# Performance work log

Measured on AMD Instinct MI355X. Metric: run time of the kernel, lower is better.

The kernel has to match this reference:

```python
import jax, jax.numpy as jnp
import numpy as np

DIM = 512
NUM_EXPERTS = 8
HID = 4 * DIM
B, S = 2, 2048


def setup_inputs() -> dict:
    key = jax.random.key(0)
    ks = jax.random.split(key, 7)
    sc = 0.02
    x = jax.random.normal(ks[0], (B, S, DIM), dtype=jnp.float32)
    Wr = jax.random.normal(ks[1], (DIM, NUM_EXPERTS), dtype=jnp.float32) * sc
    br = jnp.zeros((NUM_EXPERTS,), dtype=jnp.float32)
    W1 = jax.random.normal(ks[2], (NUM_EXPERTS, DIM, HID), dtype=jnp.float32) * sc
    b1 = jnp.zeros((NUM_EXPERTS, HID), dtype=jnp.float32)
    W2 = jax.random.normal(ks[3], (NUM_EXPERTS, HID, DIM), dtype=jnp.float32) * sc
    b2 = jnp.zeros((NUM_EXPERTS, DIM), dtype=jnp.float32)
    return {"x": x, "Wr": Wr, "br": br, "W1": W1, "b1": b1, "W2": W2, "b2": b2}


def reference(x, Wr, br, W1, b1, W2, b2):
    b, s, d = x.shape
    E = Wr.shape[1]
    xf = x.reshape(-1, d)                                   # [N, d]
    N = xf.shape[0]
    logits = xf @ Wr + br                                   # [N, E]
    probs = jax.nn.softmax(logits, axis=-1)
    top_w, top_idx = jax.lax.top_k(probs, 2)                # [N, 2]
    top_w = jax.nn.softmax(top_w, axis=-1)                  # renormalize top-2
    # combine weight per (token, expert); topk indices are distinct so add is safe
    comb = jnp.zeros((N, E), dtype=xf.dtype)
    comb = comb.at[jnp.arange(N)[:, None], top_idx].add(top_w)  # [N, E]
    # dense per-expert MLP (eval mode: dropout is identity); exact GELU as nn.GELU
    h = jax.nn.gelu(jnp.einsum('nd,edf->enf', xf, W1) + b1[:, None, :], approximate=False)
    y = jnp.einsum('enf,efd->end', h, W2) + b2[:, None, :]  # [E, N, d]
    out = jnp.einsum('end,ne->nd', y, comb)                 # weighted combine
    # load-balancing loss
    load = jnp.zeros((E,), dtype=jnp.float32).at[top_idx.reshape(-1)].add(1.0)
    load = load / load.sum()
    lb_loss = jnp.sum((load - 1.0 / E) ** 2)
    return out.reshape(b, s, d), lb_loss, load
```

## Files before the change

### kernel.cpp

```cpp
#include <hip/hip_runtime.h>
#include <hip/hip_bf16.h>

#define DIMD 512
#define NEXP 8
#define HIDN 2048
#define NTOK 4096
#define NASG 8192

typedef short bf16x8 __attribute__((ext_vector_type(8)));
typedef float f32x4 __attribute__((ext_vector_type(4)));

__device__ inline unsigned short f2bf(float f) {
  __hip_bfloat16 h = __float2bfloat16(f);
  return __builtin_bit_cast(unsigned short, h);
}

__device__ inline void gl16(const void* g, void* l) {
  __builtin_amdgcn_global_load_lds(
      (const __attribute__((address_space(1))) unsigned int*)g,
      (__attribute__((address_space(3))) unsigned int*)l, 16, 0, 0);
}

#define PIPE_WAIT4_BAR() do { \
  asm volatile("s_waitcnt vmcnt(4)" ::: "memory"); \
  __builtin_amdgcn_s_barrier(); \
  __builtin_amdgcn_sched_barrier(0); } while (0)
#define PIPE_WAIT0_BAR() do { \
  asm volatile("s_waitcnt vmcnt(0)" ::: "memory"); \
  __builtin_amdgcn_s_barrier(); \
  __builtin_amdgcn_sched_barrier(0); } while (0)
#define PIPE_POST_BAR() do { \
  asm volatile("" ::: "memory"); \
  __builtin_amdgcn_sched_barrier(0); \
  __builtin_amdgcn_s_barrier(); } while (0)

__global__ __launch_bounds__(256) void transpose_both_kernel(
    const float* __restrict__ W1, const float* __restrict__ W2,
    unsigned short* __restrict__ w1t, unsigned short* __restrict__ w2t) {
  __shared__ float tile[64][65];
  int z = blockIdx.z;
  int e = z & 7;
  const float* src; unsigned short* dst; int R, C, r0, c0;
  if (z < 8) { src = W1; dst = w1t; R = DIMD; C = HIDN; c0 = blockIdx.x * 64; r0 = blockIdx.y * 64; }
  else       { src = W2; dst = w2t; R = HIDN; C = DIMD; r0 = blockIdx.x * 64; c0 = blockIdx.y * 64; }
  const float* s = src + (size_t)e * R * C;
  unsigned short* d = dst + (size_t)e * R * C;
  for (int i = threadIdx.x; i < 4096; i += 256) {
    int r = i >> 6, c = i & 63;
    tile[r][c] = s[(size_t)(r0 + r) * C + (c0 + c)];
  }
  __syncthreads();
  for (int i = threadIdx.x; i < 2048; i += 256) {
    int c = i >> 5;
    int r = (i & 31) * 2;
    unsigned lo = f2bf(tile[r][c]);
    unsigned hi = f2bf(tile[r + 1][c]);
    *reinterpret_cast<unsigned*>(d + (size_t)(c0 + c) * R + (r0 + r)) = lo | (hi << 16);
  }
}

__global__ __launch_bounds__(256) void router_kernel(const float* __restrict__ x,
                                                     const float* __restrict__ Wr,
                                                     const float* __restrict__ br,
                                                     int* __restrict__ tidx,
                                                     float* __restrict__ tw,
                                                     unsigned short* __restrict__ xb) {
  int lane = threadIdx.x & 63;
  int n = blockIdx.x * 4 + (threadIdx.x >> 6);
  const float* xr = x + (size_t)n * DIMD;
  unsigned short* xbr = xb + (size_t)n * DIMD;
  float acc[NEXP];
#pragma unroll
  for (int e = 0; e < NEXP; ++e) acc[e] = 0.f;
#pragma unroll
  for (int it = 0; it < 2; ++it) {
    int d0 = it * 256 + lane * 4;
    float4 xv = *reinterpret_cast<const float4*>(xr + d0);
    unsigned p0 = (unsigned)f2bf(xv.x) | ((unsigned)f2bf(xv.y) << 16);
    unsigned p1 = (unsigned)f2bf(xv.z) | ((unsigned)f2bf(xv.w) << 16);
    *reinterpret_cast<uint2*>(xbr + d0) = make_uint2(p0, p1);
    const float* wr = Wr + (size_t)d0 * NEXP;
#pragma unroll
    for (int j = 0; j < 4; ++j) {
      float xj = (&xv.x)[j];
#pragma unroll
      for (int e = 0; e < NEXP; ++e) acc[e] += xj * wr[j * NEXP + e];
    }
  }
#pragma unroll
  for (int e = 0; e < NEXP; ++e) {
    float v = acc[e];
#pragma unroll
    for (int off = 32; off > 0; off >>= 1) v += __shfl_xor(v, off, 64);
    acc[e] = v + br[e];
  }
  if (lane == 0) {
    float m = acc[0];
    for (int e = 1; e < NEXP; ++e) m = fmaxf(m, acc[e]);
    float p[NEXP], s = 0.f;
    for (int e = 0; e < NEXP; ++e) { p[e] = expf(acc[e] - m); s += p[e]; }
    float inv = 1.f / s;
    for (int e = 0; e < NEXP; ++e) p[e] *= inv;
    int i0 = 0; float p0 = p[0];
    for (int e = 1; e < NEXP; ++e) if (p[e] > p0) { p0 = p[e]; i0 = e; }
    int i1 = (i0 == 0) ? 1 : 0; float p1 = p[i1];
    for (int e = 0; e < NEXP; ++e) if (e != i0 && p[e] > p1) { p1 = p[e]; i1 = e; }
    float t = expf(p1 - p0);
    float w0 = 1.f / (1.f + t);
    tidx[2 * n] = i0; tidx[2 * n + 1] = i1;
    tw[2 * n] = w0; tw[2 * n + 1] = t * w0;
  }
}

__global__ __launch_bounds__(1024) void route_pack_kernel(const int* __restrict__ tidx,
                                                          int* __restrict__ off,
                                                          int* __restrict__ list,
                                                          float* __restrict__ out_tail) {
  int tid = threadIdx.x;
  int wv = tid >> 6, lane = tid & 63;

  int ids[8];
#pragma unroll
  for (int j = 0; j < 8; ++j) ids[j] = tidx[tid * 8 + j];

  int c[NEXP];
#pragma unroll
  for (int e = 0; e < NEXP; ++e) c[e] = 0;
#pragma unroll
  for (int j = 0; j < 8; ++j)
#pragma unroll
    for (int e = 0; e < NEXP; ++e) c[e] += (ids[j] == e) ? 1 : 0;

  int inc[NEXP];
#pragma unroll
  for (int e = 0; e < NEXP; ++e) {
    int v = c[e];
#pragma unroll
    for (int d = 1; d < 64; d <<= 1) {
      int t = __shfl_up(v, d, 64);
      if (lane >= d) v += t;
    }
    inc[e] = v;
  }

  __shared__ int wtot[NEXP][16];
  __shared__ int wbase[NEXP][16];
  __shared__ int ebase[NEXP];
  if (lane == 63) {
#pragma unroll
    for (int e = 0; e < NEXP; ++e) wtot[e][wv] = inc[e];
  }
  __syncthreads();
  if (tid == 0) {
    int o = 0;
    float lb = 0.f;
    for (int e = 0; e < NEXP; ++e) {
      int s = 0;
      for (int w = 0; w < 16; ++w) { wbase[e][w] = s; s += wtot[e][w]; }
      ebase[e] = o;
      off[e] = o;
      o += s;
      float l = (float)s / (float)NASG;
      out_tail[1 + e] = l;
      float dd = l - 0.125f;
      lb += dd * dd;
    }
    off[NEXP] = o;
    out_tail[0] = lb;
  }
  __syncthreads();

  int pos[NEXP];
#pragma unroll
  for (int e = 0; e < NEXP; ++e)
    pos[e] = ebase[e] + wbase[e][wv] + (inc[e] - c[e]);

#pragma unroll
  for (int j = 0; j < 8; ++j) {
    int e = ids[j];
    int p = 0;
#pragma unroll
    for (int k = 0; k < NEXP; ++k)
      if (e == k) { p = pos[k]; pos[k] = p + 1; }
    list[p] = tid * 8 + j;
  }
}


__global__ __launch_bounds__(256) void gemm1_kernel(
    const unsigned short* __restrict__ xb,
    const unsigned short* __restrict__ w1t,
    const float* __restrict__ b1,
    const int* __restrict__ off,
    const int* __restrict__ list,
    unsigned short* __restrict__ H) {
  int e = blockIdx.x;
  int offe = off[e];
  int cnt_e = off[e + 1] - offe;
  int n0 = blockIdx.y * 128;
  int m0 = blockIdx.z * 128;
  if (m0 >= cnt_e) return;

  __shared__ char ldsb[36864];

  int tid = threadIdx.x, wv = tid >> 6, lane = tid & 63;
  int rp = lane >> 3, sl = lane & 7;
  int sx = sl ^ rp;
  int rowadd = rp * 2 + (sx >> 2);
  int kq = sx & 3;

  const unsigned short* w1e = w1t + (size_t)e * HIDN * DIMD;
  const unsigned short* asrc[2];
  const unsigned short* bsrc[2];
#pragma unroll
  for (int i = 0; i < 2; ++i) {
    int r = wv * 32 + i * 16 + rowadd;
    int rr = m0 + r;
    int tok = 0;
    if (rr < cnt_e) tok = list[offe + rr] >> 1;
    asrc[i] = xb + (size_t)tok * DIMD + kq * 8;
    bsrc[i] = w1e + (size_t)(n0 + r) * DIMD + kq * 8;
  }
  int dstA0 = wv * 2048;
  int dstA1 = wv * 2048 + 1024;

  f32x4 zero = {0.f, 0.f, 0.f, 0.f};
  f32x4 acc[4][4];
#pragma unroll
  for (int m = 0; m < 4; ++m)
#pragma unroll
    for (int n = 0; n < 4; ++n) acc[m][n] = zero;

  int wave_m = wv >> 1, wave_n = wv & 1;
  int lane16 = lane & 15, kq4 = lane >> 4;
  int ra[4], rb[4];
#pragma unroll
  for (int m = 0; m < 4; ++m) {
    int r = wave_m * 64 + m * 16 + lane16;
    ra[m] = (r >> 1) * 128 + ((((kq4 + (r & 1) * 4)) ^ ((r >> 1) & 7)) << 4);
    int rn = wave_n * 64 + m * 16 + lane16;
    rb[m] = (rn >> 1) * 128 + ((((kq4 + (rn & 1) * 4)) ^ ((rn >> 1) & 7)) << 4);
  }

  auto stage = [&](char* nb, int k0) {
    gl16(asrc[0] + k0, nb + dstA0);
    gl16(asrc[1] + k0, nb + dstA1);
    gl16(bsrc[0] + k0, nb + 8192 + dstA0);
    gl16(bsrc[1] + k0, nb + 8192 + dstA1);
  };
  auto compute = [&](const char* cb) {
    bf16x8 af[4], bfr[4];
#pragma unroll
    for (int m = 0; m < 4; ++m) af[m] = *reinterpret_cast<const bf16x8*>(cb + ra[m]);
#pragma unroll
    for (int n = 0; n < 4; ++n) bfr[n] = *reinterpret_cast<const bf16x8*>(cb + 8192 + rb[n]);
#pragma unroll
    for (int m = 0; m < 4; ++m)
#pragma unroll
      for (int n = 0; n < 4; ++n)
        acc[m][n] = __builtin_amdgcn_mfma_f32_16x16x32_bf16(af[m], bfr[n], acc[m][n], 0, 0, 0);
  };

  const int T = DIMD / 32;
  stage(ldsb, 0);
  stage(ldsb + 16384, 32);
  for (int t = 0; t < T - 2; ++t) {
    char* cb = ldsb + (t & 1) * 16384;
    PIPE_WAIT4_BAR();
    compute(cb);
    PIPE_POST_BAR();
    stage(cb, (t + 2) * 32);
  }
  PIPE_WAIT4_BAR();
  compute(ldsb + ((T - 2) & 1) * 16384);
  PIPE_POST_BAR();
  PIPE_WAIT0_BAR();
  compute(ldsb + ((T - 1) & 1) * 16384);
  PIPE_POST_BAR();

  unsigned short* Ct = (unsigned short*)ldsb;
  const float* b1e = b1 + e * HIDN;
#pragma unroll
  for (int n = 0; n < 4; ++n) {
    int cl = wave_n * 64 + n * 16 + lane16;
    float bias = b1e[n0 + cl];
#pragma unroll
    for (int m = 0; m < 4; ++m) {
#pragma unroll
      for (int q = 0; q < 4; ++q) {
        int rl = wave_m * 64 + m * 16 + kq4 * 4 + q;
        float v = acc[m][n][q] + bias;
        float g = 0.5f * v * (1.f + erff(v * 0.70710678118654752f));
        Ct[rl * 136 + cl] = f2bf(g);
      }
    }
  }
  __syncthreads();
  for (int u = tid; u < 2048; u += 256) {
    int rl = u >> 4, c8 = (u & 15) * 8;
    int r = m0 + rl;
    if (r < cnt_e) {
      uint4 v = *reinterpret_cast<const uint4*>(Ct + rl * 136 + c8);
      *reinterpret_cast<uint4*>(H + (size_t)(offe + r) * HIDN + n0 + c8) = v;
    }
  }
}

__global__ __launch_bounds__(256) void gemm2_kernel(
    const unsigned short* __restrict__ H,
    const unsigned short* __restrict__ w2t,
    const float* __restrict__ b2,
    const int* __restrict__ off,
    const int* __restrict__ list,
    const float* __restrict__ tw,
    float* __restrict__ Yw) {
  int e = blockIdx.x;
  int offe = off[e];
  int cnt_e = off[e + 1] - offe;
  int n0 = blockIdx.y * 128;
  int m0 = blockIdx.z * 128;
  if (m0 >= cnt_e) return;

  __shared__ char ldsb[32768];

  int tid = threadIdx.x, wv = tid >> 6, lane = tid & 63;
  int rp = lane >> 3, sl = lane & 7;
  int sx = sl ^ rp;
  int rowadd = rp * 2 + (sx >> 2);
  int kq = sx & 3;

  const unsigned short* w2e = w2t + (size_t)e * DIMD * HIDN;
  const unsigned short* asrc[2];
  const unsigned short* bsrc[2];
#pragma unroll
  for (int i = 0; i < 2; ++i) {
    int r = wv * 32 + i * 16 + rowadd;
    int rowa = offe + m0 + r;
    if (rowa > NASG - 1) rowa = NASG - 1;
    asrc[i] = H + (size_t)rowa * HIDN + kq * 8;
    bsrc[i] = w2e + (size_t)(n0 + r) * HIDN + kq * 8;
  }
  int dstA0 = wv * 2048;
  int dstA1 = wv * 2048 + 1024;

  f32x4 zero = {0.f, 0.f, 0.f, 0.f};
  f32x4 acc[4][4];
#pragma unroll
  for (int m = 0; m < 4; ++m)
#pragma unroll
    for (int n = 0; n < 4; ++n) acc[m][n] = zero;

  int wave_m = wv >> 1, wave_n = wv & 1;
  int lane16 = lane & 15, kq4 = lane >> 4;
  int ra[4], rb[4];
#pragma unroll
  for (int m = 0; m < 4; ++m) {
    int r = wave_m * 64 + m * 16 + lane16;
    ra[m] = (r >> 1) * 128 + ((((kq4 + (r & 1) * 4)) ^ ((r >> 1) & 7)) << 4);
    int rn = wave_n * 64 + m * 16 + lane16;
    rb[m] = (rn >> 1) * 128 + ((((kq4 + (rn & 1) * 4)) ^ ((rn >> 1) & 7)) << 4);
  }

  auto stage = [&](char* nb, int k0) {
    gl16(asrc[0] + k0, nb + dstA0);
    gl16(asrc[1] + k0, nb + dstA1);
    gl16(bsrc[0] + k0, nb + 8192 + dstA0);
    gl16(bsrc[1] + k0, nb + 8192 + dstA1);
  };
  auto compute = [&](const char* cb) {
    bf16x8 af[4], bfr[4];
#pragma unroll
    for (int m = 0; m < 4; ++m) af[m] = *reinterpret_cast<const bf16x8*>(cb + ra[m]);
#pragma unroll
    for (int n = 0; n < 4; ++n) bfr[n] = *reinterpret_cast<const bf16x8*>(cb + 8192 + rb[n]);
#pragma unroll
    for (int m = 0; m < 4; ++m)
#pragma unroll
      for (int n = 0; n < 4; ++n)
        acc[m][n] = __builtin_amdgcn_mfma_f32_16x16x32_bf16(af[m], bfr[n], acc[m][n], 0, 0, 0);
  };

  const int T = HIDN / 32;
  stage(ldsb, 0);
  stage(ldsb + 16384, 32);
  for (int t = 0; t < T - 2; ++t) {
    char* cb = ldsb + (t & 1) * 16384;
    PIPE_WAIT4_BAR();
    compute(cb);
    PIPE_POST_BAR();
    stage(cb, (t + 2) * 32);
  }
  PIPE_WAIT4_BAR();
  compute(ldsb + ((T - 2) & 1) * 16384);
  PIPE_POST_BAR();
  PIPE_WAIT0_BAR();
  compute(ldsb + ((T - 1) & 1) * 16384);
  PIPE_POST_BAR();

  const float* b2e = b2 + e * DIMD;
  float bias[4];
#pragma unroll
  for (int n = 0; n < 4; ++n) bias[n] = b2e[n0 + wave_n * 64 + n * 16 + lane16];
#pragma unroll
  for (int m = 0; m < 4; ++m) {
#pragma unroll
    for (int q = 0; q < 4; ++q) {
      int r = m0 + wave_m * 64 + m * 16 + kq4 * 4 + q;
      if (r < cnt_e) {
        int a = list[offe + r];
        float w = tw[a];
        float* yrow = Yw + (size_t)a * DIMD;
#pragma unroll
        for (int n = 0; n < 4; ++n) {
          int col = n0 + wave_n * 64 + n * 16 + lane16;
          yrow[col] = w * (acc[m][n][q] + bias[n]);
        }
      }
    }
  }
}

__global__ __launch_bounds__(256) void combine_kernel(const float* __restrict__ Yw,
                                                      float* __restrict__ out) {
  int i = (blockIdx.x * 256 + threadIdx.x) * 4;
  int n = i >> 9;
  int d = i & 511;
  float4 a = *reinterpret_cast<const float4*>(Yw + (size_t)(2 * n) * DIMD + d);
  float4 b = *reinterpret_cast<const float4*>(Yw + (size_t)(2 * n + 1) * DIMD + d);
  float4 o;
  o.x = a.x + b.x; o.y = a.y + b.y; o.z = a.z + b.z; o.w = a.w + b.w;
  *reinterpret_cast<float4*>(out + i) = o;
}

extern "C" void kernel_launch(void* const* d_in, const int* in_sizes, int n_in,
                              void* d_out, int out_size, void* d_ws, size_t ws_size,
                              hipStream_t stream) {
  const float* x  = (const float*)d_in[0];
  const float* Wr = (const float*)d_in[1];
  const float* br = (const float*)d_in[2];
  const float* W1 = (const float*)d_in[3];
  const float* b1 = (const float*)d_in[4];
  const float* W2 = (const float*)d_in[5];
  const float* b2 = (const float*)d_in[6];
  float* out = (float*)d_out;

  char* ws = (char*)d_ws;
  unsigned short* xb  = (unsigned short*)ws;  ws += (size_t)NTOK * DIMD * 2;
  unsigned short* w1t = (unsigned short*)ws;  ws += (size_t)NEXP * HIDN * DIMD * 2;
  unsigned short* w2t = (unsigned short*)ws;  ws += (size_t)NEXP * DIMD * HIDN * 2;
  unsigned short* H   = (unsigned short*)ws;  ws += (size_t)NASG * HIDN * 2;
  float* Yw = (float*)ws;                     ws += (size_t)NASG * DIMD * 4;
  float* tw = (float*)ws;                     ws += (size_t)NASG * 4;
  int* tidx = (int*)ws;                       ws += (size_t)NASG * 4;
  int* list = (int*)ws;                       ws += (size_t)NASG * 4;
  int* offp = (int*)ws;

  transpose_both_kernel<<<dim3(32, 8, 16), 256, 0, stream>>>(W1, W2, w1t, w2t);
  router_kernel<<<NTOK / 4, 256, 0, stream>>>(x, Wr, br, tidx, tw, xb);
  route_pack_kernel<<<1, 1024, 0, stream>>>(tidx, offp, list, out + (size_t)NTOK * DIMD);
  gemm1_kernel<<<dim3(NEXP, HIDN / 128, NASG / 128), 256, 0, stream>>>(xb, w1t, b1, offp, list, H);
  gemm2_kernel<<<dim3(NEXP, DIMD / 128, NASG / 128), 256, 0, stream>>>(H, w2t, b2, offp, list, tw, Yw);
  combine_kernel<<<2048, 256, 0, stream>>>(Yw, out);
}
```

Before: 118.3 us.

## Widen gemm1 N tile to 256 and vectorize weight transpose loads/stores

gemm1 now computes a 128x256 output tile per block: each wave holds 4x8 MFMA accumulators, stages four B rows per k-step and waits on vmcnt(6), and writes the GELU epilogue back through LDS in two 64-row halves. This halves how often the A (token) tiles are re-read per expert and raises MFMA work per LDS load. In exchange it uses more registers and more LDS and launches fewer blocks. The transpose kernel also switches to float4 global loads and 8-byte bf16 stores to cut memory instruction count.

Result: slower. 237.9 us (+101.2%).

```diff
diff --git a/kernel.cpp b/kernel.cpp
--- a/kernel.cpp
+++ b/kernel.cpp
@@ -21,6 +21,10 @@
       (__attribute__((address_space(3))) unsigned int*)l, 16, 0, 0);
 }
 
+#define PIPE_WAIT6_BAR() do { \
+  asm volatile("s_waitcnt vmcnt(6)" ::: "memory"); \
+  __builtin_amdgcn_s_barrier(); \
+  __builtin_amdgcn_sched_barrier(0); } while (0)
 #define PIPE_WAIT4_BAR() do { \
   asm volatile("s_waitcnt vmcnt(4)" ::: "memory"); \
   __builtin_amdgcn_s_barrier(); \
@@ -45,17 +49,18 @@
   else       { src = W2; dst = w2t; R = HIDN; C = DIMD; r0 = blockIdx.x * 64; c0 = blockIdx.y * 64; }
   const float* s = src + (size_t)e * R * C;
   unsigned short* d = dst + (size_t)e * R * C;
-  for (int i = threadIdx.x; i < 4096; i += 256) {
-    int r = i >> 6, c = i & 63;
-    tile[r][c] = s[(size_t)(r0 + r) * C + (c0 + c)];
+  for (int i = threadIdx.x; i < 1024; i += 256) {
+    int r = i >> 4, c4 = (i & 15) * 4;
+    float4 v = *reinterpret_cast<const float4*>(s + (size_t)(r0 + r) * C + (c0 + c4));
+    tile[r][c4] = v.x; tile[r][c4 + 1] = v.y; tile[r][c4 + 2] = v.z; tile[r][c4 + 3] = v.w;
   }
   __syncthreads();
-  for (int i = threadIdx.x; i < 2048; i += 256) {
-    int c = i >> 5;
-    int r = (i & 31) * 2;
-    unsigned lo = f2bf(tile[r][c]);
-    unsigned hi = f2bf(tile[r + 1][c]);
-    *reinterpret_cast<unsigned*>(d + (size_t)(c0 + c) * R + (r0 + r)) = lo | (hi << 16);
+  for (int i = threadIdx.x; i < 1024; i += 256) {
+    int c = i >> 4;
+    int r = (i & 15) * 4;
+    unsigned u0 = (unsigned)f2bf(tile[r][c]) | ((unsigned)f2bf(tile[r + 1][c]) << 16);
+    unsigned u1 = (unsigned)f2bf(tile[r + 2][c]) | ((unsigned)f2bf(tile[r + 3][c]) << 16);
+    *reinterpret_cast<uint2*>(d + (size_t)(c0 + c) * R + (r0 + r)) = make_uint2(u0, u1);
   }
 }
 
@@ -197,11 +202,11 @@
   int e = blockIdx.x;
   int offe = off[e];
   int cnt_e = off[e + 1] - offe;
-  int n0 = blockIdx.y * 128;
+  int n0 = blockIdx.y * 256;
   int m0 = blockIdx.z * 128;
   if (m0 >= cnt_e) return;
 
-  __shared__ char ldsb[36864];
+  __shared__ char ldsb[49152];
 
   int tid = threadIdx.x, wv = tid >> 6, lane = tid & 63;
   int rp = lane >> 3, sl = lane & 7;
@@ -211,7 +216,7 @@
 
   const unsigned short* w1e = w1t + (size_t)e * HIDN * DIMD;
   const unsigned short* asrc[2];
-  const unsigned short* bsrc[2];
+  const unsigned short* bsrc[4];
 #pragma unroll
   for (int i = 0; i < 2; ++i) {
     int r = wv * 32 + i * 16 + rowadd;
@@ -219,90 +224,109 @@
     int tok = 0;
     if (rr < cnt_e) tok = list[offe + rr] >> 1;
     asrc[i] = xb + (size_t)tok * DIMD + kq * 8;
+  }
+#pragma unroll
+  for (int i = 0; i < 4; ++i) {
+    int r = wv * 64 + i * 16 + rowadd;
     bsrc[i] = w1e + (size_t)(n0 + r) * DIMD + kq * 8;
   }
   int dstA0 = wv * 2048;
   int dstA1 = wv * 2048 + 1024;
+  int dstB = 8192 + wv * 4096;
 
   f32x4 zero = {0.f, 0.f, 0.f, 0.f};
-  f32x4 acc[4][4];
+  f32x4 acc[4][8];
 #pragma unroll
   for (int m = 0; m < 4; ++m)
 #pragma unroll
-    for (int n = 0; n < 4; ++n) acc[m][n] = zero;
+    for (int n = 0; n < 8; ++n) acc[m][n] = zero;
 
   int wave_m = wv >> 1, wave_n = wv & 1;
   int lane16 = lane & 15, kq4 = lane >> 4;
-  int ra[4], rb[4];
+  int ra[4], rb[8];
 #pragma unroll
   for (int m = 0; m < 4; ++m) {
     int r = wave_m * 64 + m * 16 + lane16;
     ra[m] = (r >> 1) * 128 + ((((kq4 + (r & 1) * 4)) ^ ((r >> 1) & 7)) << 4);
-    int rn = wave_n * 64 + m * 16 + lane16;
-    rb[m] = (rn >> 1) * 128 + ((((kq4 + (rn & 1) * 4)) ^ ((rn >> 1) & 7)) << 4);
+  }
+#pragma unroll
+  for (int n = 0; n < 8; ++n) {
+    int rn = wave_n * 128 + n * 16 + lane16;
+    rb[n] = (rn >> 1) * 128 + ((((kq4 + (rn & 1) * 4)) ^ ((rn >> 1) & 7)) << 4);
   }
 
   auto stage = [&](char* nb, int k0) {
     gl16(asrc[0] + k0, nb + dstA0);
     gl16(asrc[1] + k0, nb + dstA1);
-    gl16(bsrc[0] + k0, nb + 8192 + dstA0);
-    gl16(bsrc[1] + k0, nb + 8192 + dstA1);
+    gl16(bsrc[0] + k0, nb + dstB);
+    gl16(bsrc[1] + k0, nb + dstB + 1024);
+    gl16(bsrc[2] + k0, nb + dstB + 2048);
+    gl16(bsrc[3] + k0, nb + dstB + 3072);
   };
   auto compute = [&](const char* cb) {
-    bf16x8 af[4], bfr[4];
+    bf16x8 af[4], bfr[8];
 #pragma unroll
     for (int m = 0; m < 4; ++m) af[m] = *reinterpret_cast<const bf16x8*>(cb + ra[m]);
 #pragma unroll
-    for (int n = 0; n < 4; ++n) bfr[n] = *reinterpret_cast<const bf16x8*>(cb + 8192 + rb[n]);
+    for (int n = 0; n < 8; ++n) bfr[n] = *reinterpret_cast<const bf16x8*>(cb + 8192 + rb[n]);
 #pragma unroll
     for (int m = 0; m < 4; ++m)
 #pragma unroll
-      for (int n = 0; n < 4; ++n)
+      for (int n = 0; n < 8; ++n)
         acc[m][n] = __builtin_amdgcn_mfma_f32_16x16x32_bf16(af[m], bfr[n], acc[m][n], 0, 0, 0);
   };
 
   const int T = DIMD / 32;
   stage(ldsb, 0);
-  stage(ldsb + 16384, 32);
+  stage(ldsb + 24576, 32);
   for (int t = 0; t < T - 2; ++t) {
-    char* cb = ldsb + (t & 1) * 16384;
-    PIPE_WAIT4_BAR();
+    char* cb = ldsb + (t & 1) * 24576;
+    PIPE_WAIT6_BAR();
     compute(cb);
     PIPE_POST_BAR();
     stage(cb, (t + 2) * 32);
   }
-  PIPE_WAIT4_BAR();
-  compute(ldsb + ((T - 2) & 1) * 16384);
+  PIPE_WAIT6_BAR();
+  compute(ldsb + ((T - 2) & 1) * 24576);
   PIPE_POST_BAR();
   PIPE_WAIT0_BAR();
-  compute(ldsb + ((T - 1) & 1) * 16384);
+  compute(ldsb + ((T - 1) & 1) * 24576);
   PIPE_POST_BAR();
 
   unsigned short* Ct = (unsigned short*)ldsb;
   const float* b1e = b1 + e * HIDN;
-#pragma unroll
-  for (int n = 0; n < 4; ++n) {
-    int cl = wave_n * 64 + n * 16 + lane16;
-    float bias = b1e[n0 + cl];
-#pragma unroll
-    for (int m = 0; m < 4; ++m) {
-#pragma unroll
-      for (int q = 0; q < 4; ++q) {
-        int rl = wave_m * 64 + m * 16 + kq4 * 4 + q;
-        float v = acc[m][n][q] + bias;
-        float g = 0.5f * v * (1.f + erff(v * 0.70710678118654752f));
-        Ct[rl * 136 + cl] = f2bf(g);
+  float bias[8];
+#pragma unroll
+  for (int n = 0; n < 8; ++n) bias[n] = b1e[n0 + wave_n * 128 + n * 16 + lane16];
+  for (int h = 0; h < 2; ++h) {
+    if (wave_m == h) {
+#pragma unroll
+      for (int n = 0; n < 8; ++n) {
+        int cl = wave_n * 128 + n * 16 + lane16;
+#pragma unroll
+        for (int m = 0; m < 4; ++m) {
+#pragma unroll
+          for (int q = 0; q < 4; ++q) {
+            int rl = m * 16 + kq4 * 4 + q;
+            float v = acc[m][n][q] + bias[n];
+            float g = 0.5f * v * (1.f + erff(v * 0.70710678118654752f));
+            Ct[rl * 264 + cl] = f2bf(g);
+          }
+        }
       }
     }
-  }
-  __syncthreads();
-  for (int u = tid; u < 2048; u += 256) {
-    int rl = u >> 4, c8 = (u & 15) * 8;
-    int r = m0 + rl;
-    if (r < cnt_e) {
-      uint4 v = *reinterpret_cast<const uint4*>(Ct + rl * 136 + c8);
-      *reinterpret_cast<uint4*>(H + (size_t)(offe + r) * HIDN + n0 + c8) = v;
-    }
+    __syncthreads();
+#pragma unroll
+    for (int j = 0; j < 8; ++j) {
+      int u = tid + j * 256;
+      int row = u >> 5, c8 = (u & 31) * 8;
+      int r = m0 + h * 64 + row;
+      if (r < cnt_e) {
+        uint4 v = *reinterpret_cast<const uint4*>(Ct + row * 264 + c8);
+        *reinterpret_cast<uint4*>(H + (size_t)(offe + r) * HIDN + n0 + c8) = v;
+      }
+    }
+    __syncthreads();
   }
 }
 
@@ -458,7 +482,7 @@
   transpose_both_kernel<<<dim3(32, 8, 16), 256, 0, stream>>>(W1, W2, w1t, w2t);
   router_kernel<<<NTOK / 4, 256, 0, stream>>>(x, Wr, br, tidx, tw, xb);
   route_pack_kernel<<<1, 1024, 0, stream>>>(tidx, offp, list, out + (size_t)NTOK * DIMD);
-  gemm1_kernel<<<dim3(NEXP, HIDN / 128, NASG / 128), 256, 0, stream>>>(xb, w1t, b1, offp, list, H);
+  gemm1_kernel<<<dim3(NEXP, HIDN / 256, NASG / 128), 256, 0, stream>>>(xb, w1t, b1, offp, list, H);
   gemm2_kernel<<<dim3(NEXP, DIMD / 128, NASG / 128), 256, 0, stream>>>(H, w2t, b2, offp, list, tw, Yw);
   combine_kernel<<<2048, 256, 0, stream>>>(Yw, out);
 }
```

## Merge transpose and router kernels, fold combine into gemm2 via atomics

Applied to the files above, without the earlier changes.

Merges the weight transpose/convert and router into one prep kernel and widens the transpose to float4 loads and 8-byte stores. Drops the Yw buffer and combine kernel: gemm2 now atomically adds the weighted expert outputs straight into the zero-initialised output, which needs an extra memset. This removes one launch and a full fp32 intermediate round trip. The cost is many scalar fp32 atomics and a summation order that is no longer fixed.

After: 127.2 us. +7.6%, slower.

```diff
diff --git a/kernel.cpp b/kernel.cpp
--- a/kernel.cpp
+++ b/kernel.cpp
@@ -34,39 +34,40 @@
   __builtin_amdgcn_sched_barrier(0); \
   __builtin_amdgcn_s_barrier(); } while (0)
 
-__global__ __launch_bounds__(256) void transpose_both_kernel(
+__global__ __launch_bounds__(256) void prep_kernel(
     const float* __restrict__ W1, const float* __restrict__ W2,
-    unsigned short* __restrict__ w1t, unsigned short* __restrict__ w2t) {
-  __shared__ float tile[64][65];
-  int z = blockIdx.z;
-  int e = z & 7;
-  const float* src; unsigned short* dst; int R, C, r0, c0;
-  if (z < 8) { src = W1; dst = w1t; R = DIMD; C = HIDN; c0 = blockIdx.x * 64; r0 = blockIdx.y * 64; }
-  else       { src = W2; dst = w2t; R = HIDN; C = DIMD; r0 = blockIdx.x * 64; c0 = blockIdx.y * 64; }
-  const float* s = src + (size_t)e * R * C;
-  unsigned short* d = dst + (size_t)e * R * C;
-  for (int i = threadIdx.x; i < 4096; i += 256) {
-    int r = i >> 6, c = i & 63;
-    tile[r][c] = s[(size_t)(r0 + r) * C + (c0 + c)];
-  }
-  __syncthreads();
-  for (int i = threadIdx.x; i < 2048; i += 256) {
-    int c = i >> 5;
-    int r = (i & 31) * 2;
-    unsigned lo = f2bf(tile[r][c]);
-    unsigned hi = f2bf(tile[r + 1][c]);
-    *reinterpret_cast<unsigned*>(d + (size_t)(c0 + c) * R + (r0 + r)) = lo | (hi << 16);
-  }
-}
-
-__global__ __launch_bounds__(256) void router_kernel(const float* __restrict__ x,
-                                                     const float* __restrict__ Wr,
-                                                     const float* __restrict__ br,
-                                                     int* __restrict__ tidx,
-                                                     float* __restrict__ tw,
-                                                     unsigned short* __restrict__ xb) {
+    unsigned short* __restrict__ w1t, unsigned short* __restrict__ w2t,
+    const float* __restrict__ x, const float* __restrict__ Wr,
+    const float* __restrict__ br,
+    int* __restrict__ tidx, float* __restrict__ tw,
+    unsigned short* __restrict__ xb) {
+  int b = blockIdx.x;
+  if (b < 4096) {
+    __shared__ float tile[64][65];
+    int bx = b & 31, by = (b >> 5) & 7, z = b >> 8;
+    int e = z & 7;
+    const float* src; unsigned short* dst; int R, C, r0, c0;
+    if (z < 8) { src = W1; dst = w1t; R = DIMD; C = HIDN; c0 = bx * 64; r0 = by * 64; }
+    else       { src = W2; dst = w2t; R = HIDN; C = DIMD; r0 = bx * 64; c0 = by * 64; }
+    const float* s = src + (size_t)e * R * C;
+    unsigned short* d = dst + (size_t)e * R * C;
+    for (int i = threadIdx.x; i < 1024; i += 256) {
+      int r = i >> 4, c4 = (i & 15) * 4;
+      float4 v = *reinterpret_cast<const float4*>(s + (size_t)(r0 + r) * C + (c0 + c4));
+      tile[r][c4] = v.x; tile[r][c4 + 1] = v.y; tile[r][c4 + 2] = v.z; tile[r][c4 + 3] = v.w;
+    }
+    __syncthreads();
+    for (int i = threadIdx.x; i < 1024; i += 256) {
+      int c = i >> 4;
+      int r = (i & 15) * 4;
+      unsigned u0 = (unsigned)f2bf(tile[r][c]) | ((unsigned)f2bf(tile[r + 1][c]) << 16);
+      unsigned u1 = (unsigned)f2bf(tile[r + 2][c]) | ((unsigned)f2bf(tile[r + 3][c]) << 16);
+      *reinterpret_cast<uint2*>(d + (size_t)(c0 + c) * R + (r0 + r)) = make_uint2(u0, u1);
+    }
+    return;
+  }
   int lane = threadIdx.x & 63;
-  int n = blockIdx.x * 4 + (threadIdx.x >> 6);
+  int n = (b - 4096) * 4 + (threadIdx.x >> 6);
   const float* xr = x + (size_t)n * DIMD;
   unsigned short* xbr = xb + (size_t)n * DIMD;
   float acc[NEXP];
@@ -313,7 +314,7 @@
     const int* __restrict__ off,
     const int* __restrict__ list,
     const float* __restrict__ tw,
-    float* __restrict__ Yw) {
+    float* __restrict__ out) {
   int e = blockIdx.x;
   int offe = off[e];
   int cnt_e = off[e + 1] - offe;
@@ -409,27 +410,15 @@
       if (r < cnt_e) {
         int a = list[offe + r];
         float w = tw[a];
-        float* yrow = Yw + (size_t)a * DIMD;
+        float* orow = out + (size_t)(a >> 1) * DIMD;
 #pragma unroll
         for (int n = 0; n < 4; ++n) {
           int col = n0 + wave_n * 64 + n * 16 + lane16;
-          yrow[col] = w * (acc[m][n][q] + bias[n]);
+          atomicAdd(&orow[col], w * (acc[m][n][q] + bias[n]));
         }
       }
     }
   }
-}
-
-__global__ __launch_bounds__(256) void combine_kernel(const float* __restrict__ Yw,
-                                                      float* __restrict__ out) {
-  int i = (blockIdx.x * 256 + threadIdx.x) * 4;
-  int n = i >> 9;
-  int d = i & 511;
-  float4 a = *reinterpret_cast<const float4*>(Yw + (size_t)(2 * n) * DIMD + d);
-  float4 b = *reinterpret_cast<const float4*>(Yw + (size_t)(2 * n + 1) * DIMD + d);
-  float4 o;
-  o.x = a.x + b.x; o.y = a.y + b.y; o.z = a.z + b.z; o.w = a.w + b.w;
-  *reinterpret_cast<float4*>(out + i) = o;
 }
 
 extern "C" void kernel_launch(void* const* d_in, const int* in_sizes, int n_in,
@@ -449,16 +438,14 @@
   unsigned short* w1t = (unsigned short*)ws;  ws += (size_t)NEXP * HIDN * DIMD * 2;
   unsigned short* w2t = (unsigned short*)ws;  ws += (size_t)NEXP * DIMD * HIDN * 2;
   unsigned short* H   = (unsigned short*)ws;  ws += (size_t)NASG * HIDN * 2;
-  float* Yw = (float*)ws;                     ws += (size_t)NASG * DIMD * 4;
   float* tw = (float*)ws;                     ws += (size_t)NASG * 4;
   int* tidx = (int*)ws;                       ws += (size_t)NASG * 4;
   int* list = (int*)ws;                       ws += (size_t)NASG * 4;
   int* offp = (int*)ws;
 
-  transpose_both_kernel<<<dim3(32, 8, 16), 256, 0, stream>>>(W1, W2, w1t, w2t);
-  router_kernel<<<NTOK / 4, 256, 0, stream>>>(x, Wr, br, tidx, tw, xb);
+  hipMemsetAsync(out, 0, (size_t)NTOK * DIMD * 4, stream);
+  prep_kernel<<<4096 + NTOK / 4, 256, 0, stream>>>(W1, W2, w1t, w2t, x, Wr, br, tidx, tw, xb);
   route_pack_kernel<<<1, 1024, 0, stream>>>(tidx, offp, list, out + (size_t)NTOK * DIMD);
   gemm1_kernel<<<dim3(NEXP, HIDN / 128, NASG / 128), 256, 0, stream>>>(xb, w1t, b1, offp, list, H);
-  gemm2_kernel<<<dim3(NEXP, DIMD / 128, NASG / 128), 256, 0, stream>>>(H, w2t, b2, offp, list, tw, Yw);
-  combine_kernel<<<2048, 256, 0, stream>>>(Yw, out);
-}
+  gemm2_kernel<<<dim3(NEXP, DIMD / 128, NASG / 128), 256, 0, stream>>>(H, w2t, b2, offp, list, tw, out);
+}
```
